# Kernel tuning notes

Hardware: AMD Instinct MI355X
Metric: run time of the kernel (lower is better)

The kernel has to match this reference:

```python
import jax, jax.numpy as jnp
import numpy as np

NUM_HEADS = 8
NUM_LANDMARKS = 64
TOPK_LANDMARKS = 4


def setup_inputs() -> dict:
    key = jax.random.key(0)
    k1, k2, k3, k4 = jax.random.split(key, 4)
    B, N, C = 1, 2048, 512
    return {
        "x": jax.random.normal(k1, (B, N, C), jnp.float32),
        "w_qkv": jax.random.normal(k2, (3 * C, C), jnp.float32) * 0.02,
        "w_proj": jax.random.normal(k3, (C, C), jnp.float32) * 0.02,
        "b_proj": jax.random.normal(k4, (C,), jnp.float32) * 0.02,
    }


def reference(x, w_qkv, w_proj, b_proj):
    B, N, C = x.shape
    H = NUM_HEADS
    Dh = C // H
    m = min(NUM_LANDMARKS, N)          # number of segments (torch views (B,H,m,seg,D))
    kl = min(TOPK_LANDMARKS, m)
    scale = Dh ** -0.5

    qkv = (x @ w_qkv.T).reshape(B, N, 3, H, Dh).transpose(2, 0, 3, 1, 4)
    q, k, v = qkv[0], qkv[1], qkv[2]   # each (B,H,N,Dh)

    seg = -(-N // m)                   # segment length = ceil(N/m)
    pad = seg * m - N

    def segmentize(t):
        if pad > 0:
            t = jnp.pad(t, ((0, 0), (0, 0), (0, pad), (0, 0)))
        return t.reshape(B, H, m, seg, Dh)

    k_seg = segmentize(k)              # (B,H,m,seg,Dh)
    v_seg = segmentize(v)

    centroids = k_seg.mean(axis=3)     # (B,H,m,Dh) -- includes pad zeros, as in torch
    route = jnp.einsum('bhnd,bhmd->bhnm', q, centroids) * scale
    _, topk_idx = jax.lax.top_k(route, kl)  # (B,H,N,kl)

    # gather routed segments per query: (B,H,N,kl,seg,Dh)
    gather = jax.vmap(jax.vmap(lambda segs, ix: segs[ix]))
    sel_k = gather(k_seg, topk_idx).reshape(B, H, N, kl * seg, Dh)
    sel_v = gather(v_seg, topk_idx).reshape(B, H, N, kl * seg, Dh)

    attn = jnp.einsum('bhnd,bhnkd->bhnk', q, sel_k) * scale
    attn = jax.nn.softmax(attn, axis=-1)
    out = jnp.einsum('bhnk,bhnkd->bhnd', attn, sel_v)  # (B,H,N,Dh)
    out = out.transpose(0, 2, 1, 3).reshape(B, N, C)
    return out @ w_proj.T + b_proj
```

## Files before the change

kernel.cpp:

```cpp
#include <hip/hip_runtime.h>
#include <hip/hip_bf16.h>
#include <math.h>

#define N_TOK 2048
#define C_DIM 512
#define H_NUM 8
#define DH 64
#define M_LM 64
#define SEG 32
#define KL 4
#define SCALE 0.125f

typedef __attribute__((ext_vector_type(8))) short short8;
typedef __attribute__((ext_vector_type(4))) float f32x4;

__device__ inline unsigned short f2bf(float f) {
  unsigned u = __float_as_uint(f);
  u += 0x7FFF + ((u >> 16) & 1);
  return (unsigned short)(u >> 16);
}
__device__ inline float bf2f(unsigned short h) {
  return __uint_as_float(((unsigned)h) << 16);
}

__global__ __launch_bounds__(256) void gemm_qk(
    const float* __restrict__ A, const float* __restrict__ B,
    float* __restrict__ out_q, float* __restrict__ out_k)
{
  __shared__ float As[32][68];
  __shared__ float Bs[32][68];
  int tid = threadIdx.x;
  int tx = tid & 15, ty = tid >> 4;
  int row0 = blockIdx.y << 6;
  int col0 = blockIdx.x << 6;
  float acc[4][4] = {};
  int kk = tid & 31, rr = tid >> 5;

  float pa[8], pb[8];
#pragma unroll
  for (int i = 0; i < 8; i++) {
    pa[i] = A[(size_t)(row0 + rr + i * 8) * 512 + kk];
    pb[i] = B[(size_t)(col0 + rr + i * 8) * 512 + kk];
  }

  for (int k0 = 0; k0 < 512; k0 += 32) {
    __syncthreads();
#pragma unroll
    for (int i = 0; i < 8; i++) {
      As[kk][rr + i * 8] = pa[i];
      Bs[kk][rr + i * 8] = pb[i];
    }
    __syncthreads();
    if (k0 + 32 < 512) {
#pragma unroll
      for (int i = 0; i < 8; i++) {
        pa[i] = A[(size_t)(row0 + rr + i * 8) * 512 + k0 + 32 + kk];
        pb[i] = B[(size_t)(col0 + rr + i * 8) * 512 + k0 + 32 + kk];
      }
    }
#pragma unroll
    for (int kk2 = 0; kk2 < 32; kk2++) {
      float a[4], b[4];
      *(float4*)a = *(const float4*)&As[kk2][ty << 2];
      *(float4*)b = *(const float4*)&Bs[kk2][tx << 2];
#pragma unroll
      for (int i = 0; i < 4; i++)
#pragma unroll
        for (int j = 0; j < 4; j++) acc[i][j] += a[i] * b[j];
    }
  }

  int t = col0 >> 9;
  int h = (col0 >> 6) & 7;
  float* dst = (t == 0) ? out_q : out_k;
#pragma unroll
  for (int i = 0; i < 4; i++) {
    int n = row0 + (ty << 2) + i;
#pragma unroll
    for (int j = 0; j < 4; j++) {
      int d = (tx << 2) + j;
      dst[(size_t)((h << 11) + n) * DH + d] = acc[i][j];
    }
  }
}

__global__ void split3_kernel(const float* __restrict__ x, const float* __restrict__ wv,
                              const float* __restrict__ wp,
                              unsigned short* __restrict__ X2,
                              unsigned short* __restrict__ W2v,
                              unsigned short* __restrict__ WP2)
{
  int idx = blockIdx.x * 256 + threadIdx.x;
  const float* src; unsigned short* dst; int li;
  if (idx < 1048576)      { src = x;  dst = X2;  li = idx; }
  else if (idx < 1310720) { src = wv; dst = W2v; li = idx - 1048576; }
  else                    { src = wp; dst = WP2; li = idx - 1310720; }
  int r = li >> 9, k = li & 511;
  float a = src[li];
  unsigned short h1 = f2bf(a);
  float r1 = a - bf2f(h1);
  dst[(size_t)(r << 10) + k] = h1;
  dst[(size_t)(r << 10) + 512 + k] = f2bf(r1);
}

__global__ __launch_bounds__(256) void gemm_mfma(
    const unsigned short* __restrict__ A2, const unsigned short* __restrict__ B2,
    float* __restrict__ ov, float* __restrict__ ofull,
    const float* __restrict__ bias, int ldout, int mode)
{
  __shared__ short Al[4096];
  __shared__ short Bl[4096];
  int tid = threadIdx.x;
  int lane = tid & 63, w = tid >> 6;
  int row0 = blockIdx.y << 6, col0 = blockIdx.x << 6;
  int wr = (w >> 1) * 32, wc = (w & 1) * 32;
  int m_lo = tid & 7, h8 = (tid >> 3) & 7, m_hi = tid >> 6;
  int ms = m_hi * 8 + m_lo;
  int q = lane >> 4, ln = lane & 15;

  f32x4 acc[2][2];
#pragma unroll
  for (int mi = 0; mi < 2; mi++)
#pragma unroll
    for (int ni = 0; ni < 2; ni++)
#pragma unroll
      for (int r = 0; r < 4; r++) acc[mi][ni][r] = 0.0f;

  for (int s = 0; s < 24; s++) {
    int ka = (s < 8) ? s * 64 : (s < 16) ? 512 + (s - 8) * 64 : (s - 16) * 64;
    int kb = (s < 8) ? s * 64 : (s < 16) ? (s - 8) * 64 : 512 + (s - 16) * 64;
    short8 a0 = *(const short8*)(A2 + (size_t)(row0 + ms) * 1024 + ka + h8 * 8);
    short8 a1 = *(const short8*)(A2 + (size_t)(row0 + ms + 32) * 1024 + ka + h8 * 8);
    short8 b0 = *(const short8*)(B2 + (size_t)(col0 + ms) * 1024 + kb + h8 * 8);
    short8 b1 = *(const short8*)(B2 + (size_t)(col0 + ms + 32) * 1024 + kb + h8 * 8);
    __syncthreads();
    *(short8*)&Al[(h8 * 64 + ms) * 8] = a0;
    *(short8*)&Al[(h8 * 64 + ms + 32) * 8] = a1;
    *(short8*)&Bl[(h8 * 64 + ms) * 8] = b0;
    *(short8*)&Bl[(h8 * 64 + ms + 32) * 8] = b1;
    __syncthreads();
    short8 af[2][2], bf[2][2];
#pragma unroll
    for (int sub = 0; sub < 2; sub++)
#pragma unroll
      for (int i = 0; i < 2; i++) {
        af[sub][i] = *(const short8*)&Al[((sub * 4 + q) * 64 + wr + i * 16 + ln) * 8];
        bf[sub][i] = *(const short8*)&Bl[((sub * 4 + q) * 64 + wc + i * 16 + ln) * 8];
      }
#pragma unroll
    for (int sub = 0; sub < 2; sub++)
#pragma unroll
      for (int mi = 0; mi < 2; mi++)
#pragma unroll
        for (int ni = 0; ni < 2; ni++)
          acc[mi][ni] = __builtin_amdgcn_mfma_f32_16x16x32_bf16(
              af[sub][mi], bf[sub][ni], acc[mi][ni], 0, 0, 0);
  }

  if (mode == 0) {
    int hh = (col0 >> 6) & 7;
#pragma unroll
    for (int mi = 0; mi < 2; mi++)
#pragma unroll
      for (int ni = 0; ni < 2; ni++)
#pragma unroll
        for (int r = 0; r < 4; r++) {
          int row = row0 + wr + mi * 16 + q * 4 + r;
          int d = wc + ni * 16 + ln;
          ov[(size_t)((hh << 11) + row) * DH + d] = acc[mi][ni][r];
        }
  } else {
#pragma unroll
    for (int mi = 0; mi < 2; mi++)
#pragma unroll
      for (int ni = 0; ni < 2; ni++)
#pragma unroll
        for (int r = 0; r < 4; r++) {
          int row = row0 + wr + mi * 16 + q * 4 + r;
          int col = col0 + wc + ni * 16 + ln;
          ofull[(size_t)row * ldout + col] = acc[mi][ni][r] + bias[col];
        }
  }
}

__global__ void centroid_kernel(const float* __restrict__ kb, float* __restrict__ cent)
{
  int idx = blockIdx.x * blockDim.x + threadIdx.x;
  int m = (idx >> 6) & 63;
  int h = idx >> 12;
  int d = idx & 63;
  const float* base = kb + ((size_t)(h << 11) + m * SEG) * DH + d;
  float s = 0.f;
#pragma unroll
  for (int ss = 0; ss < SEG; ss++) s += base[(size_t)ss * DH];
  cent[idx] = s * (1.0f / SEG);
}

__global__ __launch_bounds__(256) void route_topk_kernel(
    const float* __restrict__ qb, const float* __restrict__ cent, int* __restrict__ topk)
{
  __shared__ float centT[64][65];
  __shared__ float qs[4][64];
  int tid = threadIdx.x;
  int wave = tid >> 6, lane = tid & 63;
  int qi = (blockIdx.x << 2) + wave;
  int h = qi >> 11;
  qs[wave][lane] = qb[(size_t)qi * DH + lane];
  const float4* c4 = (const float4*)(cent + ((size_t)h << 12));
#pragma unroll
  for (int i = 0; i < 4; i++) {
    int f4 = tid + 256 * i;
    int m = f4 >> 4;
    int d0 = (f4 & 15) * 4;
    float4 v = c4[f4];
    centT[d0][m] = v.x; centT[d0 + 1][m] = v.y;
    centT[d0 + 2][m] = v.z; centT[d0 + 3][m] = v.w;
  }
  __syncthreads();
  float dot = 0.f;
#pragma unroll
  for (int d = 0; d < 64; d++) dot += qs[wave][d] * centT[d][lane];
  float val = dot * SCALE;
  for (int r = 0; r < KL; r++) {
    float v = val;
    int id = lane;
#pragma unroll
    for (int off = 32; off; off >>= 1) {
      float ov = __shfl_xor(v, off, 64);
      int oi = __shfl_xor(id, off, 64);
      if (ov > v || (ov == v && oi < id)) { v = ov; id = oi; }
    }
    if (lane == 0) topk[qi * KL + r] = id;
    if (lane == id) val = -INFINITY;
  }
}

__global__ __launch_bounds__(256) void attn_kernel(
    const float* __restrict__ qb, const float* __restrict__ kb,
    const float* __restrict__ vb, const int* __restrict__ topk,
    unsigned short* __restrict__ ao2)
{
  __shared__ float probs[4][128];
  int tid = threadIdx.x;
  int wave = tid >> 6, lane = tid & 63;
  int qi = (blockIdx.x << 2) + wave;
  int h = qi >> 11, n = qi & 2047;
  int4 tk = *(const int4*)(topk + qi * KL);
  int segArr[4] = {tk.x, tk.y, tk.z, tk.w};
  const float* qrow = qb + (size_t)qi * DH;
  float4 qreg[4];
#pragma unroll
  for (int i = 0; i < 4; i++)
    qreg[i] = *(const float4*)(qrow + ((lane & 3) + 4 * i) * 4);

  float e[8];
  float score[8];
#pragma unroll
  for (int g = 0; g < 8; g++) {
    int seg = segArr[g >> 1];
    int key_n = seg * SEG + (lane >> 2) + 16 * (g & 1);
    const float* krow = kb + ((size_t)(h << 11) + key_n) * DH;
    float acc = 0.f;
#pragma unroll
    for (int i = 0; i < 4; i++) {
      float4 kv = *(const float4*)(krow + ((lane & 3) + 4 * i) * 4);
      float4 qv = qreg[i];
      acc += qv.x * kv.x + qv.y * kv.y + qv.z * kv.z + qv.w * kv.w;
    }
    acc += __shfl_xor(acc, 1, 64);
    acc += __shfl_xor(acc, 2, 64);
    score[g] = acc * SCALE;
  }
  float mx = score[0];
#pragma unroll
  for (int g = 1; g < 8; g++) mx = fmaxf(mx, score[g]);
#pragma unroll
  for (int off = 4; off < 64; off <<= 1) mx = fmaxf(mx, __shfl_xor(mx, off, 64));
  float ls = 0.f;
#pragma unroll
  for (int g = 0; g < 8; g++) { e[g] = expf(score[g] - mx); ls += e[g]; }
#pragma unroll
  for (int off = 4; off < 64; off <<= 1) ls += __shfl_xor(ls, off, 64);
  float inv = 1.0f / ls;
  if ((lane & 3) == 0) {
#pragma unroll
    for (int g = 0; g < 8; g++) probs[wave][(lane >> 2) + 16 * g] = e[g] * inv;
  }
  __syncthreads();

  float o = 0.f;
#pragma unroll
  for (int si = 0; si < KL; si++) {
    int seg = segArr[si];
    const float* vrow = vb + ((size_t)(h << 11) + seg * SEG) * DH + lane;
#pragma unroll
    for (int ss = 0; ss < SEG; ss++) o += probs[wave][(si << 5) + ss] * vrow[(size_t)ss * DH];
  }
  unsigned short hb = f2bf(o);
  float lo = o - bf2f(hb);
  ao2[(size_t)n * 1024 + (h << 6) + lane] = hb;
  ao2[(size_t)n * 1024 + 512 + (h << 6) + lane] = f2bf(lo);
}

extern "C" void kernel_launch(void* const* d_in, const int* in_sizes, int n_in,
                              void* d_out, int out_size, void* d_ws, size_t ws_size,
                              hipStream_t stream)
{
  const float* x      = (const float*)d_in[0];
  const float* w_qkv  = (const float*)d_in[1];
  const float* w_proj = (const float*)d_in[2];
  const float* b_proj = (const float*)d_in[3];
  float* out = (float*)d_out;

  float* base = (float*)d_ws;
  float* qbuf = base;
  float* kbuf = base + 1048576;
  float* vbuf = base + 2097152;
  float* cent = base + 3145728;
  int*   topk = (int*)(base + 3178496);
  unsigned short* X2  = (unsigned short*)(base + 3244032);
  unsigned short* W2v = (unsigned short*)(base + 4292608);
  unsigned short* WP2 = (unsigned short*)(base + 4554752);
  unsigned short* AO2 = X2;

  split3_kernel<<<6144, 256, 0, stream>>>(x, w_qkv + 1024 * 512, w_proj,
                                          X2, W2v, WP2);
  {
    dim3 grid(1024 / 64, N_TOK / 64);
    gemm_qk<<<grid, 256, 0, stream>>>(x, w_qkv, qbuf, kbuf);
  }
  {
    dim3 grid(512 / 64, N_TOK / 64);
    gemm_mfma<<<grid, 256, 0, stream>>>(X2, W2v, vbuf, nullptr, nullptr, 0, 0);
  }
  centroid_kernel<<<(H_NUM * M_LM * DH) / 256, 256, 0, stream>>>(kbuf, cent);
  route_topk_kernel<<<(H_NUM * N_TOK) / 4, 256, 0, stream>>>(qbuf, cent, topk);
  attn_kernel<<<(H_NUM * N_TOK) / 4, 256, 0, stream>>>(qbuf, kbuf, vbuf, topk, AO2);
  {
    dim3 grid(C_DIM / 64, N_TOK / 64);
    gemm_mfma<<<grid, 256, 0, stream>>>(AO2, WP2, nullptr, out, b_proj, C_DIM, 1);
  }
}
```

Measured before the change: 209.7 us.

## Bucket queries by routed segment and attend per segment with split softmax

Replaces the per-query gather attention with three steps. An atomic binning kernel groups (query, slot) pairs by head-segment. A per-segment kernel stages that segment's K/V in shared memory once and computes partial softmax and output for every query routed to it. A combine kernel then merges the four partials with log-sum-exp rescaling. The goal is to cut repeated global gathers of K/V rows, at the cost of extra launches, a memset, atomics, and an intermediate partial-output buffer that is written and read back.

```diff
diff --git a/kernel.cpp b/kernel.cpp
--- a/kernel.cpp
+++ b/kernel.cpp
@@ -235,71 +235,125 @@
   }
 }
 
-__global__ __launch_bounds__(256) void attn_kernel(
+__global__ void bin_kernel(const int* __restrict__ topk, int* __restrict__ cnt,
+                           unsigned short* __restrict__ bucket)
+{
+  int qi = blockIdx.x * 256 + threadIdx.x;
+  int4 tk = *(const int4*)(topk + qi * KL);
+  int segs[4] = {tk.x, tk.y, tk.z, tk.w};
+  int h = qi >> 11, n = qi & 2047;
+#pragma unroll
+  for (int r = 0; r < KL; r++) {
+    int hs = (h << 6) | segs[r];
+    int pos = atomicAdd(&cnt[hs], 1);
+    bucket[hs * 2048 + pos] = (unsigned short)(n | (r << 11));
+  }
+}
+
+__global__ __launch_bounds__(256) void attend_kernel(
     const float* __restrict__ qb, const float* __restrict__ kb,
-    const float* __restrict__ vb, const int* __restrict__ topk,
-    unsigned short* __restrict__ ao2)
-{
-  __shared__ float probs[4][128];
-  int tid = threadIdx.x;
-  int wave = tid >> 6, lane = tid & 63;
-  int qi = (blockIdx.x << 2) + wave;
+    const float* __restrict__ vb, const int* __restrict__ cnt,
+    const unsigned short* __restrict__ bucket,
+    float2* __restrict__ pml, float* __restrict__ po)
+{
+  __shared__ float Kl[32 * 68];
+  __shared__ float Vl[32 * 68];
+  __shared__ float qs[4][2][64];
+  __shared__ float ps[4][2][32];
+  int b = blockIdx.x;
+  int hs = b >> 2, qt = b & 3;
+  int h = hs >> 6, seg = hs & 63;
+  int tid = threadIdx.x, w = tid >> 6, lane = tid & 63;
+  {
+    int row = tid >> 3, d0 = (tid & 7) * 8;
+    const float* kr = kb + ((size_t)(h << 11) + seg * SEG + row) * DH + d0;
+    const float* vr = vb + ((size_t)(h << 11) + seg * SEG + row) * DH + d0;
+    *(float4*)&Kl[row * 68 + d0]     = *(const float4*)kr;
+    *(float4*)&Kl[row * 68 + d0 + 4] = *(const float4*)(kr + 4);
+    *(float4*)&Vl[row * 68 + d0]     = *(const float4*)vr;
+    *(float4*)&Vl[row * 68 + d0 + 4] = *(const float4*)(vr + 4);
+  }
+  __syncthreads();
+  int c = cnt[hs];
+  int k2 = lane >> 1, half = lane & 1;
+  int sid = (qt << 2) | w;
+  for (int i0 = sid * 2; i0 < c; i0 += 32) {
+    int i1 = i0 + 1;
+    bool has2 = (i1 < c);
+    int e0 = bucket[hs * 2048 + i0];
+    int e1 = has2 ? bucket[hs * 2048 + i1] : e0;
+    int n0 = e0 & 2047, r0 = (e0 >> 11) & 3;
+    int n1 = e1 & 2047, r1 = (e1 >> 11) & 3;
+    qs[w][0][lane] = qb[((size_t)(h << 11) + n0) * DH + lane];
+    qs[w][1][lane] = qb[((size_t)(h << 11) + n1) * DH + lane];
+    float a0 = 0.f, a1 = 0.f;
+#pragma unroll
+    for (int j = 0; j < 8; j++) {
+      float4 kv = *(const float4*)&Kl[k2 * 68 + half * 32 + 4 * j];
+      float4 q0 = *(const float4*)&qs[w][0][half * 32 + 4 * j];
+      float4 q1 = *(const float4*)&qs[w][1][half * 32 + 4 * j];
+      a0 += q0.x * kv.x + q0.y * kv.y + q0.z * kv.z + q0.w * kv.w;
+      a1 += q1.x * kv.x + q1.y * kv.y + q1.z * kv.z + q1.w * kv.w;
+    }
+    a0 += __shfl_xor(a0, 1, 64);
+    a1 += __shfl_xor(a1, 1, 64);
+    float s0 = a0 * SCALE, s1 = a1 * SCALE;
+    float m0 = s0, m1 = s1;
+#pragma unroll
+    for (int off = 2; off < 64; off <<= 1) {
+      m0 = fmaxf(m0, __shfl_xor(m0, off, 64));
+      m1 = fmaxf(m1, __shfl_xor(m1, off, 64));
+    }
+    float ex0 = expf(s0 - m0), ex1 = expf(s1 - m1);
+    float l0 = ex0, l1 = ex1;
+#pragma unroll
+    for (int off = 2; off < 64; off <<= 1) {
+      l0 += __shfl_xor(l0, off, 64);
+      l1 += __shfl_xor(l1, off, 64);
+    }
+    if (half == 0) { ps[w][0][k2] = ex0; ps[w][1][k2] = ex1; }
+    float o0 = 0.f, o1 = 0.f;
+#pragma unroll
+    for (int k = 0; k < 32; k++) {
+      float vv = Vl[k * 68 + lane];
+      o0 += ps[w][0][k] * vv;
+      o1 += ps[w][1][k] * vv;
+    }
+    int p0 = (((h << 11) | n0) << 2) | r0;
+    po[(size_t)p0 * 64 + lane] = o0;
+    if (lane == 0) pml[p0] = make_float2(m0, l0);
+    if (has2) {
+      int p1 = (((h << 11) | n1) << 2) | r1;
+      po[(size_t)p1 * 64 + lane] = o1;
+      if (lane == 0) pml[p1] = make_float2(m1, l1);
+    }
+  }
+}
+
+__global__ void combine_kernel(const float2* __restrict__ pml,
+                               const float* __restrict__ po,
+                               unsigned short* __restrict__ ao2)
+{
+  int idx = blockIdx.x * 256 + threadIdx.x;
+  int d = idx & 63;
+  int qi = idx >> 6;
   int h = qi >> 11, n = qi & 2047;
-  int4 tk = *(const int4*)(topk + qi * KL);
-  int segArr[4] = {tk.x, tk.y, tk.z, tk.w};
-  const float* qrow = qb + (size_t)qi * DH;
-  float4 qreg[4];
-#pragma unroll
-  for (int i = 0; i < 4; i++)
-    qreg[i] = *(const float4*)(qrow + ((lane & 3) + 4 * i) * 4);
-
-  float e[8];
-  float score[8];
-#pragma unroll
-  for (int g = 0; g < 8; g++) {
-    int seg = segArr[g >> 1];
-    int key_n = seg * SEG + (lane >> 2) + 16 * (g & 1);
-    const float* krow = kb + ((size_t)(h << 11) + key_n) * DH;
-    float acc = 0.f;
-#pragma unroll
-    for (int i = 0; i < 4; i++) {
-      float4 kv = *(const float4*)(krow + ((lane & 3) + 4 * i) * 4);
-      float4 qv = qreg[i];
-      acc += qv.x * kv.x + qv.y * kv.y + qv.z * kv.z + qv.w * kv.w;
-    }
-    acc += __shfl_xor(acc, 1, 64);
-    acc += __shfl_xor(acc, 2, 64);
-    score[g] = acc * SCALE;
-  }
-  float mx = score[0];
-#pragma unroll
-  for (int g = 1; g < 8; g++) mx = fmaxf(mx, score[g]);
-#pragma unroll
-  for (int off = 4; off < 64; off <<= 1) mx = fmaxf(mx, __shfl_xor(mx, off, 64));
-  float ls = 0.f;
-#pragma unroll
-  for (int g = 0; g < 8; g++) { e[g] = expf(score[g] - mx); ls += e[g]; }
-#pragma unroll
-  for (int off = 4; off < 64; off <<= 1) ls += __shfl_xor(ls, off, 64);
-  float inv = 1.0f / ls;
-  if ((lane & 3) == 0) {
-#pragma unroll
-    for (int g = 0; g < 8; g++) probs[wave][(lane >> 2) + 16 * g] = e[g] * inv;
-  }
-  __syncthreads();
-
-  float o = 0.f;
-#pragma unroll
-  for (int si = 0; si < KL; si++) {
-    int seg = segArr[si];
-    const float* vrow = vb + ((size_t)(h << 11) + seg * SEG) * DH + lane;
-#pragma unroll
-    for (int ss = 0; ss < SEG; ss++) o += probs[wave][(si << 5) + ss] * vrow[(size_t)ss * DH];
-  }
+  float2 ml0 = pml[qi * 4 + 0], ml1 = pml[qi * 4 + 1];
+  float2 ml2 = pml[qi * 4 + 2], ml3 = pml[qi * 4 + 3];
+  float M = fmaxf(fmaxf(ml0.x, ml1.x), fmaxf(ml2.x, ml3.x));
+  float w0 = expf(ml0.x - M), w1 = expf(ml1.x - M);
+  float w2 = expf(ml2.x - M), w3 = expf(ml3.x - M);
+  float L = w0 * ml0.y + w1 * ml1.y + w2 * ml2.y + w3 * ml3.y;
+  float o = w0 * po[(size_t)(qi * 4 + 0) * 64 + d]
+          + w1 * po[(size_t)(qi * 4 + 1) * 64 + d]
+          + w2 * po[(size_t)(qi * 4 + 2) * 64 + d]
+          + w3 * po[(size_t)(qi * 4 + 3) * 64 + d];
+  o /= L;
   unsigned short hb = f2bf(o);
-  float lo = o - bf2f(hb);
-  ao2[(size_t)n * 1024 + (h << 6) + lane] = hb;
-  ao2[(size_t)n * 1024 + 512 + (h << 6) + lane] = f2bf(lo);
+  unsigned short lb = f2bf(o - bf2f(hb));
+  size_t off0 = (size_t)n * 1024 + (h << 6) + d;
+  ao2[off0] = hb;
+  ao2[off0 + 512] = lb;
 }
 
 extern "C" void kernel_launch(void* const* d_in, const int* in_sizes, int n_in,
@@ -322,6 +376,10 @@
   unsigned short* W2v = (unsigned short*)(base + 4292608);
   unsigned short* WP2 = (unsigned short*)(base + 4554752);
   unsigned short* AO2 = X2;
+  int* cnt = (int*)(base + 4816896);
+  unsigned short* bucket = (unsigned short*)(base + 4817408);
+  float2* pml = (float2*)(base + 5341696);
+  float* po   = base + 5472768;
 
   split3_kernel<<<6144, 256, 0, stream>>>(x, w_qkv + 1024 * 512, w_proj,
                                           X2, W2v, WP2);
@@ -335,7 +393,10 @@
   }
   centroid_kernel<<<(H_NUM * M_LM * DH) / 256, 256, 0, stream>>>(kbuf, cent);
   route_topk_kernel<<<(H_NUM * N_TOK) / 4, 256, 0, stream>>>(qbuf, cent, topk);
-  attn_kernel<<<(H_NUM * N_TOK) / 4, 256, 0, stream>>>(qbuf, kbuf, vbuf, topk, AO2);
+  hipMemsetAsync(cnt, 0, 512 * sizeof(int), stream);
+  bin_kernel<<<64, 256, 0, stream>>>(topk, cnt, bucket);
+  attend_kernel<<<2048, 256, 0, stream>>>(qbuf, kbuf, vbuf, cnt, bucket, pml, po);
+  combine_kernel<<<4096, 256, 0, stream>>>(pml, po, AO2);
   {
     dim3 grid(C_DIM / 64, N_TOK / 64);
     gemm_mfma<<<grid, 256, 0, stream>>>(AO2, WP2, nullptr, out, b_proj, C_DIM, 1);
```

Result: slower. 226.0 us (+7.8%).
